# Kernel tuning notes

Measured on AMD Instinct MI355X. Metric: run time of the kernel, lower is better.

Reference implementation:

```python
import jax, jax.numpy as jnp
import numpy as np

GAMMA = 0.99
LAMBDA = 0.95
NU = 0.001
LOG_2PI = float(np.log(2.0 * np.pi))

B, T, H, R, C, A = 256, 64, 512, 32, 32, 64
H1, H2 = 1024, 1024
D = H + R * C  # critic input dim = hidden_state + flattened latent


def setup_inputs() -> dict:
    key = jax.random.key(0)
    ks = jax.random.split(key, 13)
    sc = lambda n: 1.0 / np.sqrt(n)
    return {
        "h": jax.random.normal(ks[0], (B, T, H), jnp.float32),
        "z": jax.random.normal(ks[1], (B, T, R, C), jnp.float32),
        "reward": jax.random.normal(ks[2], (B, T, 1), jnp.float32) * 0.1,
        "cont": jax.random.uniform(ks[3], (B, T, 1), jnp.float32),
        "action": jax.random.normal(ks[4], (B, T, A), jnp.float32),
        "a_mu": jax.random.normal(ks[5], (B, T, A), jnp.float32),
        "a_sigma": jax.random.uniform(ks[6], (B, T, A), jnp.float32) + 0.5,
        "W1": jax.random.normal(ks[7], (D, H1), jnp.float32) * sc(D),
        "b1": jnp.zeros((H1,), jnp.float32),
        "W2": jax.random.normal(ks[8], (H1, H2), jnp.float32) * sc(H1),
        "b2": jnp.zeros((H2,), jnp.float32),
        "W3": jax.random.normal(ks[9], (H2, 1), jnp.float32) * sc(H2),
        "b3": jnp.zeros((1,), jnp.float32),
    }


def _critic(h, z, W1, b1, W2, b2, W3, b3):
    # flatten latent [B,T,R,C] -> [B,T,R*C], concat with hidden state
    zf = z.reshape(z.shape[0], z.shape[1], -1)
    st = jnp.concatenate([h, zf], axis=-1)  # [B,T,D]
    x = jax.nn.silu(st @ W1 + b1)
    x = jax.nn.silu(x @ W2 + b2)
    return x @ W3 + b3  # [B,T,1]


def _r_lambda(value, reward, cont):
    # value/reward/cont: [B,T,1]; backward TD(lambda) recursion over time
    vt = value[..., 0].T   # [T,B] time-major
    rt = reward[..., 0].T
    ct = cont[..., 0].T

    def step(R_next, xs):
        r, c, v_next = xs
        R_cur = r + GAMMA * c * ((1.0 - LAMBDA) * v_next + LAMBDA * R_next)
        return R_cur, R_cur

    _, Rs = jax.lax.scan(step, vt[-1], (rt[:-1], ct[:-1], vt[1:]), reverse=True)
    R_lam = jnp.concatenate([Rs, vt[-1:]], axis=0)  # [T,B]
    return R_lam.T[..., None]  # [B,T,1]


def reference(h, z, reward, cont, action, a_mu, a_sigma, W1, b1, W2, b2, W3, b3):
    value = _critic(h, z, W1, b1, W2, b2, W3, b3)  # [B,T,1]
    # R_lambda uses detached value estimates
    R_lam = _r_lambda(jax.lax.stop_gradient(value), reward, cont)  # [B,T,1]
    advantage = R_lam - value  # [B,T,1]

    # Normal(mu, sigma) log_prob and entropy
    log_sig = jnp.log(a_sigma)
    log_prob = -0.5 * jnp.square((action - a_mu) / a_sigma) - log_sig - 0.5 * LOG_2PI  # [B,T,A]
    entropy = 0.5 + 0.5 * LOG_2PI + log_sig  # [B,T,A]

    loss_actor = -jnp.mean(
        log_prob * jax.lax.stop_gradient(advantage)
        + NU * jax.lax.stop_gradient(entropy)
    )
    loss_critic = jnp.mean(0.5 * jnp.square(value - jax.lax.stop_gradient(R_lam)))
    return jnp.stack([loss_actor, loss_critic])
```

## Files before the change

### kernel.cpp

```cpp
#include <hip/hip_runtime.h>
#include <hip/hip_bf16.h>
#include <stdint.h>

typedef short s8v  __attribute__((ext_vector_type(8)));
typedef float f4v  __attribute__((ext_vector_type(4)));

__device__ __forceinline__ unsigned short f2bf(float f) {
  unsigned int u = __float_as_uint(f);
  u += 0x7fffu + ((u >> 16) & 1u);
  return (unsigned short)(u >> 16);
}

#define GLOAD16(g, l)                                                          \
  __builtin_amdgcn_global_load_lds(                                            \
      (const __attribute__((address_space(1))) unsigned int*)(g),              \
      (__attribute__((address_space(3))) unsigned int*)(l), 16, 0, 0)

__global__ __launch_bounds__(256) void prep_x(const float* __restrict__ h,
                                              const float* __restrict__ z,
                                              unsigned short* __restrict__ X) {
  int idx = blockIdx.x * 256 + threadIdx.x;
  int m = idx / 192;
  int c = (idx - m * 192) * 8;
  const float* s = (c < 512) ? (h + (size_t)m * 512 + c)
                             : (z + (size_t)m * 1024 + (c - 512));
  f4v f0 = *(const f4v*)s;
  f4v f1 = *(const f4v*)(s + 4);
  s8v o;
  o[0] = (short)f2bf(f0[0]); o[1] = (short)f2bf(f0[1]);
  o[2] = (short)f2bf(f0[2]); o[3] = (short)f2bf(f0[3]);
  o[4] = (short)f2bf(f1[0]); o[5] = (short)f2bf(f1[1]);
  o[6] = (short)f2bf(f1[2]); o[7] = (short)f2bf(f1[3]);
  *(s8v*)(X + (size_t)m * 1536 + c) = o;
}

__global__ __launch_bounds__(256) void transpose_w(const float* __restrict__ W,
                                                   unsigned short* __restrict__ WT,
                                                   int K, int N) {
  __shared__ float tile[32][33];
  int tx = threadIdx.x & 31;
  int ty = threadIdx.x >> 5;
  int k0 = blockIdx.x * 32;
  int n0 = blockIdx.y * 32;
#pragma unroll
  for (int i = 0; i < 4; ++i)
    tile[ty + i * 8][tx] = W[(size_t)(k0 + ty + i * 8) * N + n0 + tx];
  __syncthreads();
#pragma unroll
  for (int i = 0; i < 4; ++i)
    WT[(size_t)(n0 + ty + i * 8) * K + k0 + tx] = f2bf(tile[tx][ty + i * 8]);
}

template<int K, bool FUSE>
__global__ __launch_bounds__(512) void gemm256(
    const unsigned short* __restrict__ A, const unsigned short* __restrict__ Bt,
    const float* __restrict__ bias, unsigned short* __restrict__ Cout,
    const float* __restrict__ W3, float* __restrict__ value) {
  constexpr int NOUT = 1024;
  constexpr int NT = K / 64;
  __shared__ char lds[131072];

  const int tid = threadIdx.x;
  const int w = tid >> 6, l = tid & 63;
  const int wr = w >> 2, wc = w & 3;
  const int tm = blockIdx.x * 256;
  const int tn = blockIdx.y * 256;
  const int l15 = l & 15, lh = l >> 4;

  const int srow = tid >> 3;
  const int sk = ((tid & 7) ^ (srow & 7)) * 8;
  const unsigned short* Ag = A  + (size_t)(tm + srow) * K + sk;
  const unsigned short* Bg = Bt + (size_t)(tn + srow) * K + sk;
  const int wb = w * 1024;

  auto stage_ht = [&](int p, char* bufbase, int kt) {
    const unsigned short* g =
        (p < 2 ? Ag : Bg) + (size_t)(p & 1) * 128 * K + kt;
    char* d = bufbase + p * 16384 + wb;
    GLOAD16(g, d);
    GLOAD16(g + (size_t)64 * K, d + 8192);
  };

  f4v acc[8][4];
#pragma unroll
  for (int i = 0; i < 8; ++i)
#pragma unroll
    for (int j = 0; j < 4; ++j) acc[i][j] = (f4v){0.f, 0.f, 0.f, 0.f};

#pragma unroll
  for (int p = 0; p < 4; ++p) stage_ht(p, lds, 0);
  asm volatile("s_waitcnt vmcnt(0)" ::: "memory");
  __builtin_amdgcn_s_barrier();

  s8v bf[4];
  for (int t = 0; t < NT; ++t) {
    char* const cb = lds + ((t & 1) ? 65536 : 0);
    char* const nb = lds + ((t & 1) ? 0 : 65536);
    char* const Ab = cb;
    char* const Bb = cb + 32768;
    const bool st = (t + 1 < NT);
    const int nkt = (t + 1) * 64;
#pragma unroll
    for (int ph = 0; ph < 4; ++ph) {
      const int kk = ph >> 1, mh = ph & 1;
      const int k16 = kk * 4 + lh;
      if (mh == 0) {
#pragma unroll
        for (int ni = 0; ni < 4; ++ni) {
          const int row = wc * 64 + ni * 16 + l15;
          bf[ni] = *(const s8v*)(Bb + row * 128 + ((k16 ^ (row & 7)) << 4));
        }
      }
      s8v af[4];
#pragma unroll
      for (int mi = 0; mi < 4; ++mi) {
        const int row = wr * 128 + (mh * 4 + mi) * 16 + l15;
        af[mi] = *(const s8v*)(Ab + row * 128 + ((k16 ^ (row & 7)) << 4));
      }
      if (st) stage_ht(ph, nb, nkt);
      __builtin_amdgcn_s_barrier();
      __builtin_amdgcn_s_setprio(1);
#pragma unroll
      for (int mi = 0; mi < 4; ++mi)
#pragma unroll
        for (int ni = 0; ni < 4; ++ni)
          acc[mh * 4 + mi][ni] = __builtin_amdgcn_mfma_f32_16x16x32_bf16(
              af[mi], bf[ni], acc[mh * 4 + mi][ni], 0, 0, 0);
      __builtin_amdgcn_s_setprio(0);
      if (ph == 3)
        asm volatile("s_waitcnt vmcnt(0)" ::: "memory");
      __builtin_amdgcn_s_barrier();
    }
  }

  if constexpr (!FUSE) {
#pragma unroll
    for (int ni = 0; ni < 4; ++ni) {
      const int col = tn + wc * 64 + ni * 16 + l15;
      const float bb = bias[col];
#pragma unroll
      for (int mi = 0; mi < 8; ++mi) {
#pragma unroll
        for (int r = 0; r < 4; ++r) {
          const int row = tm + wr * 128 + mi * 16 + lh * 4 + r;
          float v = acc[mi][ni][r] + bb;
          v = v / (1.f + __expf(-v));
          Cout[(size_t)row * NOUT + col] = f2bf(v);
        }
      }
    }
  } else {
    float bb[4], w3[4];
#pragma unroll
    for (int ni = 0; ni < 4; ++ni) {
      const int col = tn + wc * 64 + ni * 16 + l15;
      bb[ni] = bias[col];
      w3[ni] = W3[col];
    }
#pragma unroll
    for (int mi = 0; mi < 8; ++mi) {
#pragma unroll
      for (int r = 0; r < 4; ++r) {
        float s = 0.f;
#pragma unroll
        for (int ni = 0; ni < 4; ++ni) {
          float v = acc[mi][ni][r] + bb[ni];
          v = v / (1.f + __expf(-v));
          s += v * w3[ni];
        }
        s += __shfl_xor(s, 1);
        s += __shfl_xor(s, 2);
        s += __shfl_xor(s, 4);
        s += __shfl_xor(s, 8);
        if (l15 == 0)
          atomicAdd(&value[tm + wr * 128 + mi * 16 + lh * 4 + r], s);
      }
    }
  }
}

__global__ __launch_bounds__(256) void td_actor(
    const float* __restrict__ value, const float* __restrict__ reward,
    const float* __restrict__ cont, const float* __restrict__ b3,
    const float* __restrict__ action, const float* __restrict__ a_mu,
    const float* __restrict__ a_sigma, float* __restrict__ accs) {
  __shared__ float vv[64], rr[64], cc[64], adv_s[64];
  const int b = blockIdx.x, tid = threadIdx.x;
  if (tid < 64) {
    vv[tid] = value[b * 64 + tid] + b3[0];
    rr[tid] = reward[b * 64 + tid];
    cc[tid] = cont[b * 64 + tid];
  }
  __syncthreads();
  if (tid == 0) {
    const float g = 0.99f, lam = 0.95f;
    float Rn = vv[63];
    adv_s[63] = 0.f;
    float s2 = 0.f;
    for (int t = 62; t >= 0; --t) {
      float R = rr[t] + g * cc[t] * ((1.f - lam) * vv[t + 1] + lam * Rn);
      float a = R - vv[t];
      adv_s[t] = a;
      s2 += a * a;
      Rn = R;
    }
    atomicAdd(&accs[0], s2);
  }
  __syncthreads();
  const float C1 = 0.91893853320467274f;
  const float NU = 0.001f;
  const float av = adv_s[tid >> 2];
  const size_t base = (size_t)b * 4096 + tid * 16;
  float s = 0.f;
#pragma unroll
  for (int j = 0; j < 4; ++j) {
    f4v a  = *(const f4v*)(action  + base + j * 4);
    f4v mu = *(const f4v*)(a_mu    + base + j * 4);
    f4v sg = *(const f4v*)(a_sigma + base + j * 4);
#pragma unroll
    for (int i = 0; i < 4; ++i) {
      float d = (a[i] - mu[i]) / sg[i];
      float ls = __logf(sg[i]);
      float lp = -0.5f * d * d - ls - C1;
      s += lp * av + NU * (0.5f + C1 + ls);
    }
  }
#pragma unroll
  for (int off = 32; off; off >>= 1) s += __shfl_down(s, off);
  __shared__ float red[4];
  if ((tid & 63) == 0) red[tid >> 6] = s;
  __syncthreads();
  if (tid == 0) atomicAdd(&accs[1], red[0] + red[1] + red[2] + red[3]);
}

__global__ void fin_kernel(const float* __restrict__ accs, float* __restrict__ out) {
  out[0] = -accs[1] / 1048576.0f;
  out[1] = 0.5f * accs[0] / 16384.0f;
}

extern "C" void kernel_launch(void* const* d_in, const int* in_sizes, int n_in,
                              void* d_out, int out_size, void* d_ws, size_t ws_size,
                              hipStream_t stream) {
  const float* h       = (const float*)d_in[0];
  const float* z       = (const float*)d_in[1];
  const float* reward  = (const float*)d_in[2];
  const float* cont    = (const float*)d_in[3];
  const float* action  = (const float*)d_in[4];
  const float* a_mu    = (const float*)d_in[5];
  const float* a_sigma = (const float*)d_in[6];
  const float* W1      = (const float*)d_in[7];
  const float* b1      = (const float*)d_in[8];
  const float* W2      = (const float*)d_in[9];
  const float* b2      = (const float*)d_in[10];
  const float* W3      = (const float*)d_in[11];
  const float* b3      = (const float*)d_in[12];

  char* ws = (char*)d_ws;
  unsigned short* X   = (unsigned short*)(ws);
  unsigned short* W1T = (unsigned short*)(ws + 50331648);
  unsigned short* W2T = (unsigned short*)(ws + 53477376);
  unsigned short* X1  = (unsigned short*)(ws + 55574528);
  float* value = (float*)(ws + 89128960);
  float* accs  = (float*)(ws + 89194496);

  hipMemsetAsync(value, 0, 65552, stream);
  prep_x<<<12288, 256, 0, stream>>>(h, z, X);
  transpose_w<<<dim3(48, 32), 256, 0, stream>>>(W1, W1T, 1536, 1024);
  transpose_w<<<dim3(32, 32), 256, 0, stream>>>(W2, W2T, 1024, 1024);
  gemm256<1536, false><<<dim3(64, 4), 512, 0, stream>>>(X, W1T, b1, X1, nullptr, nullptr);
  gemm256<1024, true><<<dim3(64, 4), 512, 0, stream>>>(X1, W2T, b2, nullptr, W3, value);
  td_actor<<<256, 256, 0, stream>>>(value, reward, cont, b3, action, a_mu, a_sigma, accs);
  fin_kernel<<<1, 1, 0, stream>>>(accs, (float*)d_out);
}
```

Measured before the change: 273.4 us.

## Switch GEMM to 4-buffer K=32 pipeline with 3-tile prefetch depth

Restructures the bf16 MFMA GEMM main loop. K-tiles shrink from 64 to 32 and LDS is split into four 32KB buffers, with three tiles in flight via global_load_lds and vmcnt-based waits. The old per-phase double barrier is replaced by one barrier per tile. The LDS row/swizzle layout is remapped so each 128-byte row holds two matrix rows of 32 k-elements. This aims to hide global load latency and cut barrier stalls, at the cost of twice as many iterations, each doing less MFMA work per barrier, and more fragile vmcnt accounting.

Result: faster. 265.3 us (-3.0%).

```diff
diff --git a/kernel.cpp b/kernel.cpp
--- a/kernel.cpp
+++ b/kernel.cpp
@@ -57,7 +57,7 @@
     const float* __restrict__ bias, unsigned short* __restrict__ Cout,
     const float* __restrict__ W3, float* __restrict__ value) {
   constexpr int NOUT = 1024;
-  constexpr int NT = K / 64;
+  constexpr int NT = K / 32;
   __shared__ char lds[131072];
 
   const int tid = threadIdx.x;
@@ -67,71 +67,73 @@
   const int tn = blockIdx.y * 256;
   const int l15 = l & 15, lh = l >> 4;
 
-  const int srow = tid >> 3;
-  const int sk = ((tid & 7) ^ (srow & 7)) * 8;
+  const int ul   = (tid & 7) ^ ((tid >> 3) & 7);
+  const int srow = ((tid >> 3) << 1) + (ul >> 2);
+  const int sk   = (ul & 3) * 8;
   const unsigned short* Ag = A  + (size_t)(tm + srow) * K + sk;
   const unsigned short* Bg = Bt + (size_t)(tn + srow) * K + sk;
   const int wb = w * 1024;
 
-  auto stage_ht = [&](int p, char* bufbase, int kt) {
-    const unsigned short* g =
-        (p < 2 ? Ag : Bg) + (size_t)(p & 1) * 128 * K + kt;
-    char* d = bufbase + p * 16384 + wb;
-    GLOAD16(g, d);
-    GLOAD16(g + (size_t)64 * K, d + 8192);
+  const int ra = wr * 128 + l15;
+  const int rb = wc * 64 + l15;
+  const int aoff = (ra >> 1) * 128 + (((((ra & 1) << 2) | lh) ^ ((ra >> 1) & 7)) << 4);
+  const int boff = 16384 + (rb >> 1) * 128 + (((((rb & 1) << 2) | lh) ^ ((rb >> 1) & 7)) << 4);
+
+  f4v acc[8][4];
+#pragma unroll
+  for (int i = 0; i < 8; ++i)
+#pragma unroll
+    for (int j = 0; j < 4; ++j) acc[i][j] = (f4v){0.f, 0.f, 0.f, 0.f};
+
+  auto stage = [&](int t) {
+    char* d = lds + (t & 3) * 32768 + wb;
+    const int kt = t * 32;
+    GLOAD16(Ag + kt, d);
+    GLOAD16(Ag + (size_t)128 * K + kt, d + 8192);
+    GLOAD16(Bg + kt, d + 16384);
+    GLOAD16(Bg + (size_t)128 * K + kt, d + 24576);
   };
 
-  f4v acc[8][4];
-#pragma unroll
-  for (int i = 0; i < 8; ++i)
-#pragma unroll
-    for (int j = 0; j < 4; ++j) acc[i][j] = (f4v){0.f, 0.f, 0.f, 0.f};
-
-#pragma unroll
-  for (int p = 0; p < 4; ++p) stage_ht(p, lds, 0);
-  asm volatile("s_waitcnt vmcnt(0)" ::: "memory");
-  __builtin_amdgcn_s_barrier();
-
-  s8v bf[4];
-  for (int t = 0; t < NT; ++t) {
-    char* const cb = lds + ((t & 1) ? 65536 : 0);
-    char* const nb = lds + ((t & 1) ? 0 : 65536);
-    char* const Ab = cb;
-    char* const Bb = cb + 32768;
-    const bool st = (t + 1 < NT);
-    const int nkt = (t + 1) * 64;
-#pragma unroll
-    for (int ph = 0; ph < 4; ++ph) {
-      const int kk = ph >> 1, mh = ph & 1;
-      const int k16 = kk * 4 + lh;
-      if (mh == 0) {
-#pragma unroll
-        for (int ni = 0; ni < 4; ++ni) {
-          const int row = wc * 64 + ni * 16 + l15;
-          bf[ni] = *(const s8v*)(Bb + row * 128 + ((k16 ^ (row & 7)) << 4));
-        }
-      }
-      s8v af[4];
-#pragma unroll
-      for (int mi = 0; mi < 4; ++mi) {
-        const int row = wr * 128 + (mh * 4 + mi) * 16 + l15;
-        af[mi] = *(const s8v*)(Ab + row * 128 + ((k16 ^ (row & 7)) << 4));
-      }
-      if (st) stage_ht(ph, nb, nkt);
-      __builtin_amdgcn_s_barrier();
-      __builtin_amdgcn_s_setprio(1);
-#pragma unroll
-      for (int mi = 0; mi < 4; ++mi)
-#pragma unroll
-        for (int ni = 0; ni < 4; ++ni)
-          acc[mh * 4 + mi][ni] = __builtin_amdgcn_mfma_f32_16x16x32_bf16(
-              af[mi], bf[ni], acc[mh * 4 + mi][ni], 0, 0, 0);
-      __builtin_amdgcn_s_setprio(0);
-      if (ph == 3)
-        asm volatile("s_waitcnt vmcnt(0)" ::: "memory");
-      __builtin_amdgcn_s_barrier();
-    }
-  }
+  stage(0); stage(1); stage(2);
+
+#define MFMA4(mi, av)                                                          \
+  acc[mi][0] = __builtin_amdgcn_mfma_f32_16x16x32_bf16(av, bf0, acc[mi][0], 0, 0, 0); \
+  acc[mi][1] = __builtin_amdgcn_mfma_f32_16x16x32_bf16(av, bf1, acc[mi][1], 0, 0, 0); \
+  acc[mi][2] = __builtin_amdgcn_mfma_f32_16x16x32_bf16(av, bf2, acc[mi][2], 0, 0, 0); \
+  acc[mi][3] = __builtin_amdgcn_mfma_f32_16x16x32_bf16(av, bf3, acc[mi][3], 0, 0, 0);
+
+#define TILE(t, VM)                                                            \
+  {                                                                            \
+    asm volatile(VM ::: "memory");                                             \
+    __builtin_amdgcn_s_barrier();                                              \
+    char* const sb = lds + ((t) & 3) * 32768;                                  \
+    s8v bf0 = *(const s8v*)(sb + boff);                                        \
+    s8v bf1 = *(const s8v*)(sb + boff + 1024);                                 \
+    s8v bf2 = *(const s8v*)(sb + boff + 2048);                                 \
+    s8v bf3 = *(const s8v*)(sb + boff + 3072);                                 \
+    s8v a0 = *(const s8v*)(sb + aoff);                                         \
+    s8v a1 = *(const s8v*)(sb + aoff + 1024);                                  \
+    s8v a2 = *(const s8v*)(sb + aoff + 2048);                                  \
+    s8v a3 = *(const s8v*)(sb + aoff + 3072);                                  \
+    if ((t) + 3 < NT) stage((t) + 3);                                          \
+    __builtin_amdgcn_s_setprio(1);                                             \
+    MFMA4(0, a0) MFMA4(1, a1) MFMA4(2, a2) MFMA4(3, a3)                        \
+    __builtin_amdgcn_s_setprio(0);                                             \
+    a0 = *(const s8v*)(sb + aoff + 4096);                                      \
+    a1 = *(const s8v*)(sb + aoff + 5120);                                      \
+    a2 = *(const s8v*)(sb + aoff + 6144);                                      \
+    a3 = *(const s8v*)(sb + aoff + 7168);                                      \
+    __builtin_amdgcn_s_setprio(1);                                             \
+    MFMA4(4, a0) MFMA4(5, a1) MFMA4(6, a2) MFMA4(7, a3)                        \
+    __builtin_amdgcn_s_setprio(0);                                             \
+  }
+
+  for (int t = 0; t < NT - 2; ++t) TILE(t, "s_waitcnt vmcnt(8)")
+  TILE(NT - 2, "s_waitcnt vmcnt(4)")
+  TILE(NT - 1, "s_waitcnt vmcnt(0)")
+
+#undef TILE
+#undef MFMA4
 
   if constexpr (!FUSE) {
 #pragma unroll
```
